# Performance work log

Measured on AMD Instinct MI355X. Metric: run time of the kernel, lower is better.

Reference implementation:

```python
import jax, jax.numpy as jnp
import numpy as np

EMBED = 1024
HEADS = 16
HEAD_DIM = EMBED // HEADS
N, SEQ = 8, 1024


def setup_inputs() -> dict:
    key = jax.random.key(0)
    ks = jax.random.split(key, 8)
    s = 1.0 / np.sqrt(HEAD_DIM)
    so = 1.0 / np.sqrt(EMBED)
    return {
        "values": jax.random.normal(ks[0], (N, SEQ, EMBED), jnp.float32),
        "keys": jax.random.normal(ks[1], (N, SEQ, EMBED), jnp.float32),
        "query": jax.random.normal(ks[2], (N, SEQ, EMBED), jnp.float32),
        "mask": jnp.ones((N, 1, 1, SEQ), jnp.int32),
        "Wv": jax.random.normal(ks[3], (HEAD_DIM, HEAD_DIM), jnp.float32) * s,
        "Wk": jax.random.normal(ks[4], (HEAD_DIM, HEAD_DIM), jnp.float32) * s,
        "Wq": jax.random.normal(ks[5], (HEAD_DIM, HEAD_DIM), jnp.float32) * s,
        "Wo": jax.random.normal(ks[6], (EMBED, EMBED), jnp.float32) * so,
        "bo": jnp.zeros((EMBED,), jnp.float32),
    }


def reference(values, keys, query, mask, Wv, Wk, Wq, Wo, bo):
    n, ql = query.shape[0], query.shape[1]
    # split heads: (N, L, H, D)
    v = values.reshape(n, -1, HEADS, HEAD_DIM)
    k = keys.reshape(n, -1, HEADS, HEAD_DIM)
    q = query.reshape(n, -1, HEADS, HEAD_DIM)
    # per-head linear projections (nn.Linear, no bias): x @ W^T
    v = jnp.einsum("nlhd,ed->nlhe", v, Wv)
    k = jnp.einsum("nlhd,ed->nlhe", k, Wk)
    q = jnp.einsum("nlhd,ed->nlhe", q, Wq)
    # scores: (N, H, Q, K)
    energy = jnp.einsum("nqhd,nkhd->nhqk", q, k)
    energy = jnp.where(mask == 0, jnp.float32(-1e10), energy)
    attn = jax.nn.softmax(energy / jnp.sqrt(jnp.float32(EMBED)), axis=-1)
    out = jnp.einsum("nhqk,nkhd->nqhd", attn, v).reshape(n, ql, EMBED)
    return out @ Wo.T + bo
```

## Files before the change

kernel.cpp:

```cpp
#include <hip/hip_runtime.h>
#include <hip/hip_bf16.h>
#include <stdint.h>

typedef unsigned short u16;
typedef __bf16 bf16_t;
typedef bf16_t bf16x8 __attribute__((ext_vector_type(8)));
typedef float f32x4 __attribute__((ext_vector_type(4)));
typedef float f32x16 __attribute__((ext_vector_type(16)));

#define MFMA16(a, b, c) __builtin_amdgcn_mfma_f32_16x16x32_bf16((a), (b), (c), 0, 0, 0)
#define MFMA32(a, b, c) __builtin_amdgcn_mfma_f32_32x32x16_bf16((a), (b), (c), 0, 0, 0)

#define NBATCH 8
#define SEQL 1024
#define EMB 1024
#define NHEAD 16
#define HD 64

static __device__ __forceinline__ u16 f2b(float f) {
  bf16_t b = (bf16_t)f;
  return __builtin_bit_cast(u16, b);
}

union V16 { uint4 u; bf16x8 b; };

static __device__ __forceinline__ bf16x8 ldb8(const u16* p) {
  V16 v; v.u = *(const uint4*)p; return v.b;
}

static __device__ __forceinline__ bf16x8 cvt8(const float* p) {
  float4 a = *(const float4*)p;
  float4 b = *(const float4*)(p + 4);
  bf16x8 r;
  r[0] = (bf16_t)a.x; r[1] = (bf16_t)a.y; r[2] = (bf16_t)a.z; r[3] = (bf16_t)a.w;
  r[4] = (bf16_t)b.x; r[5] = (bf16_t)b.y; r[6] = (bf16_t)b.z; r[7] = (bf16_t)b.w;
  return r;
}

static __device__ __forceinline__ void gload16(const void* g, void* l) {
  __builtin_amdgcn_global_load_lds((__attribute__((address_space(1))) void*)(uintptr_t)g,
                                   (__attribute__((address_space(3))) void*)l, 16, 0, 0);
}

static __device__ __forceinline__ unsigned cvtpk(float lo, float hi) {
  unsigned r;
  asm("v_cvt_pk_bf16_f32 %0, %1, %2" : "=v"(r) : "v"(lo), "v"(hi));
  return r;
}

static __device__ __forceinline__ f32x16 zero16() {
  f32x16 z;
#pragma unroll
  for (int i = 0; i < 16; ++i) z[i] = 0.f;
  return z;
}

__global__ __launch_bounds__(256) void k_wcvt(const float* __restrict__ Wo, u16* __restrict__ Wob) {
  int i = (blockIdx.x * 256 + threadIdx.x) * 4;
  float4 f = *(const float4*)(Wo + i);
  unsigned p0 = (unsigned)f2b(f.x) | ((unsigned)f2b(f.y) << 16);
  unsigned p1 = (unsigned)f2b(f.z) | ((unsigned)f2b(f.w) << 16);
  uint2 o; o.x = p0; o.y = p1;
  *(uint2*)(Wob + i) = o;
}

__global__ __launch_bounds__(256) void k_proj3(const float* __restrict__ Xv, const float* __restrict__ Xk,
                                               const float* __restrict__ Xq, const float* __restrict__ Wv,
                                               const float* __restrict__ Wk, const float* __restrict__ Wq,
                                               u16* __restrict__ Vt, u16* __restrict__ Kp, u16* __restrict__ Qp) {
  __shared__ __align__(16) u16 sbuf[4608];
  int z = blockIdx.z;
  const float* X = (z == 0) ? Xv : (z == 1) ? Xk : Xq;
  const float* W = (z == 0) ? Wv : (z == 1) ? Wk : Wq;
  u16* Out = (z == 0) ? Vt : (z == 1) ? Kp : Qp;
  int vmode = (z == 0);
  float qs = (z == 2) ? 0.04508422f : 1.0f;

  int nh = blockIdx.x;
  int n = nh >> 4, h = nh & 15;
  int tid = threadIdx.x, w = tid >> 6, lane = tid & 63;
  int lr = lane & 15, lg = lane >> 4;

  bf16x8 bw[4][2];
#pragma unroll
  for (int c = 0; c < 4; ++c)
#pragma unroll
    for (int kk = 0; kk < 2; ++kk)
      bw[c][kk] = cvt8(W + (lr + 16 * c) * HD + kk * 32 + lg * 8);

#pragma unroll 1
  for (int it = 0; it < 4; ++it) {
    int rowblk = (blockIdx.y * 4 + it) * 4 + w;
    int l = rowblk * 16 + lr;
    const float* xp = X + ((size_t)(n * SEQL + l)) * EMB + h * HD + lg * 8;
    bf16x8 a0 = cvt8(xp);
    bf16x8 a1 = cvt8(xp + 32);
    f32x4 acc[4];
#pragma unroll
    for (int c = 0; c < 4; ++c) {
      f32x4 z4 = {0.f, 0.f, 0.f, 0.f};
      z4 = MFMA16(a0, bw[c][0], z4);
      z4 = MFMA16(a1, bw[c][1], z4);
      acc[c] = z4;
    }
    if (!vmode) {
      u16* ob = sbuf + w * 1152;
#pragma unroll
      for (int c = 0; c < 4; ++c)
#pragma unroll
        for (int rr = 0; rr < 4; ++rr)
          ob[(lg * 4 + rr) * 72 + lr + 16 * c] = f2b(acc[c][rr] * qs);
      int orow = lane >> 2, oseg = lane & 3;
      uint4 v0 = *(const uint4*)(ob + orow * 72 + oseg * 16);
      uint4 v1 = *(const uint4*)(ob + orow * 72 + oseg * 16 + 8);
      u16* dst = Out + ((size_t)nh * SEQL + rowblk * 16 + orow) * HD + oseg * 16;
      *(uint4*)dst = v0;
      *(uint4*)(dst + 8) = v1;
    } else {
#pragma unroll
      for (int c = 0; c < 4; ++c)
#pragma unroll
        for (int rr = 0; rr < 4; ++rr)
          sbuf[(lr + 16 * c) * 72 + w * 16 + lg * 4 + rr] = f2b(acc[c][rr]);
      __syncthreads();
      int d = tid >> 2, seg = tid & 3;
      uint4 v0 = *(const uint4*)(sbuf + d * 72 + seg * 16);
      uint4 v1 = *(const uint4*)(sbuf + d * 72 + seg * 16 + 8);
      int lchunk = (blockIdx.y * 4 + it) * 64;
      u16* dst = Out + ((size_t)nh * HD + d) * SEQL + lchunk + seg * 16;
      *(uint4*)dst = v0;
      *(uint4*)(dst + 8) = v1;
      __syncthreads();
    }
  }
}

__global__ __launch_bounds__(256, 2) void k_attn2(const u16* __restrict__ Qp, const u16* __restrict__ Kp,
                                                  const u16* __restrict__ Vt, const int* __restrict__ mask,
                                                  u16* __restrict__ AO) {
  __shared__ __align__(16) u16 SMEM[2][8192];
  __shared__ unsigned long long mkb[16];
  __shared__ __align__(16) float winv[4][2][32];

  int nh = blockIdx.x;
  int n = nh >> 4, h = nh & 15;
  int tid = threadIdx.x, w = tid >> 6, lane = tid & 63;
  int q = lane & 31, hi = lane >> 5;
  int q0w = blockIdx.y * 256 + w * 64;

  bf16x8 bq[2][4];
#pragma unroll
  for (int g = 0; g < 2; ++g) {
    const u16* qbase = Qp + ((size_t)nh * SEQL + q0w + g * 32 + q) * HD + hi * 8;
#pragma unroll
    for (int kk = 0; kk < 4; ++kk) bq[g][kk] = ldb8(qbase + kk * 16);
  }

  const u16* gK = Kp + (size_t)nh * SEQL * HD;
  const u16* gV = Vt + (size_t)nh * HD * SEQL;
  int sr = lane >> 3, sslot = lane & 7;

  auto STAGE = [&](int b, int t) {
#pragma unroll
    for (int j = 0; j < 2; ++j) {
      int r = 16 * w + 8 * j + sr;
      int slot = sslot ^ (r & 7);
      gload16(gK + ((size_t)(t * 64 + r)) * HD + slot * 8,
              &SMEM[b][w * 1024 + j * 512]);
      gload16(gV + (size_t)r * SEQL + t * 64 + slot * 8,
              &SMEM[b][4096 + w * 1024 + j * 512]);
    }
  };

  STAGE(0, 0);
#pragma unroll 1
  for (int t = w; t < 16; t += 4) {
    int mv = mask[n * SEQL + t * 64 + lane];
    unsigned long long b = __ballot(mv != 0);
    if (lane == 0) mkb[t] = b;
  }
  __syncthreads();

  f32x16 oacc[2][2];
  oacc[0][0] = zero16(); oacc[0][1] = zero16();
  oacc[1][0] = zero16(); oacc[1][1] = zero16();
  float lsum0 = 0.f, lsum1 = 0.f;
  int buf = 0;

#pragma unroll 1
  for (int kt = 0; kt < 16; ++kt) {
    if (kt < 15) STAGE(buf ^ 1, kt + 1);
    const u16* KB = &SMEM[buf][0];
    const u16* VB = &SMEM[buf][4096];
    unsigned long long mb = mkb[kt];

#pragma unroll
    for (int c = 0; c < 2; ++c) {
      f32x16 s0 = zero16(), s1 = zero16();
      {
        int row = 32 * c + q;
        int swz = (row & 7) << 3;
        const u16* kr = KB + row * 64;
        __builtin_amdgcn_s_setprio(1);
#pragma unroll
        for (int kk = 0; kk < 4; ++kk) {
          bf16x8 ak = ldb8(kr + ((16 * kk + 8 * hi) ^ swz));
          s0 = MFMA32(ak, bq[0][kk], s0);
          s1 = MFMA32(ak, bq[1][kk], s1);
        }
        __builtin_amdgcn_s_setprio(0);
      }

#pragma unroll
      for (int rr = 0; rr < 16; ++rr) {
        s0[rr] = __builtin_amdgcn_exp2f(s0[rr]);
        s1[rr] = __builtin_amdgcn_exp2f(s1[rr]);
      }
      if (mb != ~0ull) {
#pragma unroll
        for (int rr = 0; rr < 16; ++rr) {
          int kpos = 32 * c + 4 * hi + (rr & 3) + 8 * (rr >> 2);
          if (!((mb >> kpos) & 1)) { s0[rr] = 0.f; s1[rr] = 0.f; }
        }
      }
#pragma unroll
      for (int rr = 0; rr < 16; ++rr) { lsum0 += s0[rr]; lsum1 += s1[rr]; }

      bf16x8 pa0[2], pa1[2];
#pragma unroll
      for (int p2 = 0; p2 < 2; ++p2) {
        unsigned a0 = cvtpk(s0[8 * p2 + 0], s0[8 * p2 + 1]);
        unsigned a1 = cvtpk(s0[8 * p2 + 2], s0[8 * p2 + 3]);
        unsigned b0 = cvtpk(s0[8 * p2 + 4], s0[8 * p2 + 5]);
        unsigned b1 = cvtpk(s0[8 * p2 + 6], s0[8 * p2 + 7]);
        auto r0 = __builtin_amdgcn_permlane32_swap(a0, b0, false, false);
        auto r1 = __builtin_amdgcn_permlane32_swap(a1, b1, false, false);
        union { unsigned u[4]; bf16x8 v; } pu;
        pu.u[0] = r0[0]; pu.u[1] = r1[0]; pu.u[2] = r0[1]; pu.u[3] = r1[1];
        pa0[p2] = pu.v;
        unsigned c0 = cvtpk(s1[8 * p2 + 0], s1[8 * p2 + 1]);
        unsigned c1 = cvtpk(s1[8 * p2 + 2], s1[8 * p2 + 3]);
        unsigned d0 = cvtpk(s1[8 * p2 + 4], s1[8 * p2 + 5]);
        unsigned d1 = cvtpk(s1[8 * p2 + 6], s1[8 * p2 + 7]);
        auto r2 = __builtin_amdgcn_permlane32_swap(c0, d0, false, false);
        auto r3 = __builtin_amdgcn_permlane32_swap(c1, d1, false, false);
        union { unsigned u[4]; bf16x8 v; } pv;
        pv.u[0] = r2[0]; pv.u[1] = r3[0]; pv.u[2] = r2[1]; pv.u[3] = r3[1];
        pa1[p2] = pv.v;
      }

      __builtin_amdgcn_s_setprio(1);
#pragma unroll
      for (int cp = 0; cp < 2; ++cp) {
        int row = 32 * cp + q;
        int swz = (row & 7) << 3;
        const u16* vr = VB + row * 64;
#pragma unroll
        for (int p2 = 0; p2 < 2; ++p2) {
          int t = 2 * c + p2;
          bf16x8 vb = ldb8(vr + ((16 * t + 8 * hi) ^ swz));
          oacc[0][cp] = MFMA32(pa0[p2], vb, oacc[0][cp]);
          oacc[1][cp] = MFMA32(pa1[p2], vb, oacc[1][cp]);
        }
      }
      __builtin_amdgcn_s_setprio(0);
    }
    __syncthreads();
    buf ^= 1;
  }

  float t0 = lsum0 + __shfl_xor(lsum0, 32);
  float t1 = lsum1 + __shfl_xor(lsum1, 32);
  if (!hi) { winv[w][0][q] = 1.0f / t0; winv[w][1][q] = 1.0f / t1; }

  u16* ob = &SMEM[0][0] + w * 2560;
  int orow = lane >> 1, ohalf = lane & 1;
#pragma unroll
  for (int g = 0; g < 2; ++g) {
    float iq[16];
#pragma unroll
    for (int w2 = 0; w2 < 4; ++w2) {
      float4 f = *(const float4*)&winv[w][g][8 * w2 + 4 * hi];
      iq[4 * w2 + 0] = f.x; iq[4 * w2 + 1] = f.y; iq[4 * w2 + 2] = f.z; iq[4 * w2 + 3] = f.w;
    }
#pragma unroll
    for (int cp = 0; cp < 2; ++cp)
#pragma unroll
      for (int rr = 0; rr < 16; ++rr) {
        int qr = (rr & 3) + 8 * (rr >> 2) + 4 * hi;
        ob[qr * 80 + 32 * cp + q] = f2b(oacc[g][cp][rr] * iq[rr]);
      }
    __builtin_amdgcn_s_barrier();
    const u16* srcp = ob + orow * 80 + ohalf * 32;
    uint4 v0 = *(const uint4*)srcp;
    uint4 v1 = *(const uint4*)(srcp + 8);
    uint4 v2 = *(const uint4*)(srcp + 16);
    uint4 v3 = *(const uint4*)(srcp + 24);
    u16* dst = AO + ((size_t)(n * SEQL + q0w + g * 32 + orow)) * EMB + h * HD + ohalf * 32;
    *(uint4*)dst = v0;
    *(uint4*)(dst + 8) = v1;
    *(uint4*)(dst + 16) = v2;
    *(uint4*)(dst + 24) = v3;
  }
}

__global__ __launch_bounds__(256) void k_out(const u16* __restrict__ AO, const u16* __restrict__ Wob,
                                             const float* __restrict__ bo, float* __restrict__ Y) {
  __shared__ __align__(16) u16 As[2][4096];
  __shared__ __align__(16) u16 Bs[2][4096];
  int n0 = blockIdx.x * 128, m0 = blockIdx.y * 128;
  int tid = threadIdx.x, w = tid >> 6, lane = tid & 63;
  int lr = lane & 15, lg = lane >> 4;
  int wr = w >> 1, wc = w & 1;
  int srow = lane >> 2, sseg = lane & 3;

  auto STAGE = [&](int b, int kb) {
#pragma unroll
    for (int j = 0; j < 2; ++j) {
      int row = 32 * w + 16 * j + srow;
      gload16(AO + (size_t)(m0 + row) * EMB + kb * 32 + sseg * 8, &As[b][w * 1024 + j * 512]);
      gload16(Wob + (size_t)(n0 + row) * EMB + kb * 32 + sseg * 8, &Bs[b][w * 1024 + j * 512]);
    }
  };

  f32x4 acc[4][4] = {};
  STAGE(0, 0);
  __syncthreads();
  int buf = 0;
#pragma unroll 1
  for (int kb = 0; kb < 32; ++kb) {
    if (kb < 31) STAGE(buf ^ 1, kb + 1);
    bf16x8 a[4], b[4];
#pragma unroll
    for (int mi = 0; mi < 4; ++mi)
      a[mi] = ldb8(&As[buf][(wr * 64 + mi * 16 + lr) * 32 + lg * 8]);
#pragma unroll
    for (int ni = 0; ni < 4; ++ni)
      b[ni] = ldb8(&Bs[buf][(wc * 64 + ni * 16 + lr) * 32 + lg * 8]);
#pragma unroll
    for (int mi = 0; mi < 4; ++mi)
#pragma unroll
      for (int ni = 0; ni < 4; ++ni)
        acc[mi][ni] = MFMA16(a[mi], b[ni], acc[mi][ni]);
    __syncthreads();
    buf ^= 1;
  }
#pragma unroll
  for (int ni = 0; ni < 4; ++ni) {
    float bov = bo[n0 + wc * 64 + ni * 16 + lr];
#pragma unroll
    for (int mi = 0; mi < 4; ++mi) {
#pragma unroll
      for (int rr = 0; rr < 4; ++rr) {
        int row = m0 + wr * 64 + mi * 16 + lg * 4 + rr;
        int col = n0 + wc * 64 + ni * 16 + lr;
        Y[(size_t)row * EMB + col] = acc[mi][ni][rr] + bov;
      }
    }
  }
}

extern "C" void kernel_launch(void* const* d_in, const int* in_sizes, int n_in,
                              void* d_out, int out_size, void* d_ws, size_t ws_size,
                              hipStream_t stream) {
  (void)in_sizes; (void)n_in; (void)out_size; (void)ws_size;
  const float* values = (const float*)d_in[0];
  const float* keys   = (const float*)d_in[1];
  const float* query  = (const float*)d_in[2];
  const int*   mask   = (const int*)d_in[3];
  const float* Wv = (const float*)d_in[4];
  const float* Wk = (const float*)d_in[5];
  const float* Wq = (const float*)d_in[6];
  const float* Wo = (const float*)d_in[7];
  const float* bo = (const float*)d_in[8];
  float* out = (float*)d_out;

  u16* ws  = (u16*)d_ws;
  u16* Qp  = ws;
  u16* Kp  = ws + (size_t)8 * 1024 * 1024;
  u16* Vt  = ws + (size_t)16 * 1024 * 1024;
  u16* AO  = ws + (size_t)24 * 1024 * 1024;
  u16* Wob = ws + (size_t)32 * 1024 * 1024;

  k_wcvt<<<dim3(1024), dim3(256), 0, stream>>>(Wo, Wob);
  k_proj3<<<dim3(128, 4, 3), dim3(256), 0, stream>>>(values, keys, query, Wv, Wk, Wq, Vt, Kp, Qp);
  k_attn2<<<dim3(128, 4), dim3(256), 0, stream>>>(Qp, Kp, Vt, mask, AO);
  k_out<<<dim3(8, 64), dim3(256), 0, stream>>>(AO, Wob, bo, out);
}
```

Before: 116.8 us.

## Tile projection by contiguous row blocks and store V in blocked layout

The projection kernel now has each block load 16 full contiguous rows of the fp32 input (all heads) into swizzled shared memory, and each wave then projects four heads from that tile. Before, each block strided through one head's 64-column slice of many rows. The V output switches from a transposed [d][seq] layout to a blocked layout of 8 sequence positions by 64 dims. This drops the block-wide syncthreads in the V path, and the attention kernel's V staging addresses are updated to match. The aim is fully coalesced global reads of the large fp32 inputs and cheaper V writes, at the cost of more shared memory per block (about 43 KB), which may reduce occupancy.

```diff
diff --git a/kernel.cpp b/kernel.cpp
--- a/kernel.cpp
+++ b/kernel.cpp
@@ -68,7 +68,9 @@
                                                const float* __restrict__ Xq, const float* __restrict__ Wv,
                                                const float* __restrict__ Wk, const float* __restrict__ Wq,
                                                u16* __restrict__ Vt, u16* __restrict__ Kp, u16* __restrict__ Qp) {
-  __shared__ __align__(16) u16 sbuf[4608];
+  __shared__ __align__(16) u16 xs[16 * 1024];
+  __shared__ __align__(16) u16 obuf[4][16 * 72];
+  __shared__ __align__(16) u16 ob2[4][1024];
   int z = blockIdx.z;
   const float* X = (z == 0) ? Xv : (z == 1) ? Xk : Xq;
   const float* W = (z == 0) ? Wv : (z == 1) ? Wk : Wq;
@@ -76,8 +78,8 @@
   int vmode = (z == 0);
   float qs = (z == 2) ? 0.04508422f : 1.0f;
 
-  int nh = blockIdx.x;
-  int n = nh >> 4, h = nh & 15;
+  int gr0 = blockIdx.x * 16;
+  int n = gr0 >> 10, l0 = gr0 & 1023;
   int tid = threadIdx.x, w = tid >> 6, lane = tid & 63;
   int lr = lane & 15, lg = lane >> 4;
 
@@ -88,23 +90,31 @@
     for (int kk = 0; kk < 2; ++kk)
       bw[c][kk] = cvt8(W + (lr + 16 * c) * HD + kk * 32 + lg * 8);
 
+#pragma unroll
+  for (int i = 0; i < 8; ++i) {
+    int m = i * 256 + tid;
+    int row = m >> 7, cc = m & 127;
+    V16 v; v.b = cvt8(X + (size_t)gr0 * 1024 + (size_t)m * 8);
+    *(uint4*)(xs + row * 1024 + ((cc ^ (row & 7)) * 8)) = v.u;
+  }
+  __syncthreads();
+
 #pragma unroll 1
-  for (int it = 0; it < 4; ++it) {
-    int rowblk = (blockIdx.y * 4 + it) * 4 + w;
-    int l = rowblk * 16 + lr;
-    const float* xp = X + ((size_t)(n * SEQL + l)) * EMB + h * HD + lg * 8;
-    bf16x8 a0 = cvt8(xp);
-    bf16x8 a1 = cvt8(xp + 32);
+  for (int h4 = 0; h4 < 4; ++h4) {
+    int h = w * 4 + h4;
+    int nh = n * 16 + h;
+    bf16x8 a0 = ldb8(xs + lr * 1024 + (((h * 8 + 0 + lg) ^ (lr & 7)) * 8));
+    bf16x8 a1 = ldb8(xs + lr * 1024 + (((h * 8 + 4 + lg) ^ (lr & 7)) * 8));
     f32x4 acc[4];
 #pragma unroll
     for (int c = 0; c < 4; ++c) {
-      f32x4 z4 = {0.f, 0.f, 0.f, 0.f};
-      z4 = MFMA16(a0, bw[c][0], z4);
-      z4 = MFMA16(a1, bw[c][1], z4);
-      acc[c] = z4;
+      f32x4 zz = {0.f, 0.f, 0.f, 0.f};
+      zz = MFMA16(a0, bw[c][0], zz);
+      zz = MFMA16(a1, bw[c][1], zz);
+      acc[c] = zz;
     }
     if (!vmode) {
-      u16* ob = sbuf + w * 1152;
+      u16* ob = obuf[w];
 #pragma unroll
       for (int c = 0; c < 4; ++c)
 #pragma unroll
@@ -113,24 +123,23 @@
       int orow = lane >> 2, oseg = lane & 3;
       uint4 v0 = *(const uint4*)(ob + orow * 72 + oseg * 16);
       uint4 v1 = *(const uint4*)(ob + orow * 72 + oseg * 16 + 8);
-      u16* dst = Out + ((size_t)nh * SEQL + rowblk * 16 + orow) * HD + oseg * 16;
+      u16* dst = Out + ((size_t)nh * SEQL + l0 + orow) * HD + oseg * 16;
       *(uint4*)dst = v0;
       *(uint4*)(dst + 8) = v1;
     } else {
-#pragma unroll
-      for (int c = 0; c < 4; ++c)
-#pragma unroll
-        for (int rr = 0; rr < 4; ++rr)
-          sbuf[(lr + 16 * c) * 72 + w * 16 + lg * 4 + rr] = f2b(acc[c][rr]);
-      __syncthreads();
-      int d = tid >> 2, seg = tid & 3;
-      uint4 v0 = *(const uint4*)(sbuf + d * 72 + seg * 16);
-      uint4 v1 = *(const uint4*)(sbuf + d * 72 + seg * 16 + 8);
-      int lchunk = (blockIdx.y * 4 + it) * 64;
-      u16* dst = Out + ((size_t)nh * HD + d) * SEQL + lchunk + seg * 16;
-      *(uint4*)dst = v0;
-      *(uint4*)(dst + 8) = v1;
-      __syncthreads();
+      u16* o2 = ob2[w];
+#pragma unroll
+      for (int c = 0; c < 4; ++c) {
+        ushort4 p;
+        p.x = f2b(acc[c][0]); p.y = f2b(acc[c][1]); p.z = f2b(acc[c][2]); p.w = f2b(acc[c][3]);
+        *(ushort4*)(o2 + (lg >> 1) * 512 + (lr + 16 * c) * 8 + (lg & 1) * 4) = p;
+      }
+      int lb0 = l0 >> 3;
+#pragma unroll
+      for (int lbi = 0; lbi < 2; ++lbi) {
+        uint4 vv = *(const uint4*)(o2 + lbi * 512 + lane * 8);
+        *(uint4*)(Out + (size_t)nh * 65536 + (size_t)(lb0 + lbi) * 512 + lane * 8) = vv;
+      }
     }
   }
 }
@@ -167,7 +176,7 @@
       int slot = sslot ^ (r & 7);
       gload16(gK + ((size_t)(t * 64 + r)) * HD + slot * 8,
               &SMEM[b][w * 1024 + j * 512]);
-      gload16(gV + (size_t)r * SEQL + t * 64 + slot * 8,
+      gload16(gV + (size_t)(t * 8 + slot) * 512 + r * 8,
               &SMEM[b][4096 + w * 1024 + j * 512]);
     }
   };
@@ -383,7 +392,7 @@
   u16* Wob = ws + (size_t)32 * 1024 * 1024;
 
   k_wcvt<<<dim3(1024), dim3(256), 0, stream>>>(Wo, Wob);
-  k_proj3<<<dim3(128, 4, 3), dim3(256), 0, stream>>>(values, keys, query, Wv, Wk, Wq, Vt, Kp, Qp);
+  k_proj3<<<dim3(512, 1, 3), dim3(256), 0, stream>>>(values, keys, query, Wv, Wk, Wq, Vt, Kp, Qp);
   k_attn2<<<dim3(128, 4), dim3(256), 0, stream>>>(Qp, Kp, Vt, mask, AO);
   k_out<<<dim3(8, 64), dim3(256), 0, stream>>>(AO, Wob, bo, out);
 }
```

Measured after the change: 106.8 us. 8.6% less time.
